# Optimization experiments

Hardware: AMD Instinct MI355X
Metric: run time of the kernel (lower is better)

The kernel has to match this reference:

```python
import jax, jax.numpy as jnp
import numpy as np

NUM_HEADS = 12


def setup_inputs() -> dict:
    key = jax.random.key(0)
    ks = jax.random.split(key, 9)
    R, C, B, E = 128, 256, 1, 768
    s = 1.0 / np.sqrt(E)
    return {
        "x": jax.random.normal(ks[0], (R, C, B, E), jnp.float32),
        "wq": jax.random.normal(ks[1], (E, E), jnp.float32) * s,
        "bq": jax.random.normal(ks[2], (E,), jnp.float32) * 0.02,
        "wk": jax.random.normal(ks[3], (E, E), jnp.float32) * s,
        "bk": jax.random.normal(ks[4], (E,), jnp.float32) * 0.02,
        "wv": jax.random.normal(ks[5], (E, E), jnp.float32) * s,
        "bv": jax.random.normal(ks[6], (E,), jnp.float32) * 0.02,
        "wo": jax.random.normal(ks[7], (E, E), jnp.float32) * s,
        "bo": jax.random.normal(ks[8], (E,), jnp.float32) * 0.02,
    }


def reference(x, wq, bq, wk, bk, wv, bv, wo, bo):
    R, C, B, E = x.shape
    H = NUM_HEADS
    D = E // H
    # scaling = head_dim^-0.5 / sqrt(num_rows)  (tied row attention)
    scaling = (D ** -0.5) / jnp.sqrt(jnp.asarray(R, x.dtype))
    q = (x @ wq + bq).reshape(R, C, B, H, D) * scaling
    k = (x @ wk + bk).reshape(R, C, B, H, D)
    v = (x @ wv + bv).reshape(R, C, B, H, D)
    # tied attention: contract QK^T over rows as well as head_dim
    attn_weights = jnp.einsum('ribhd,rjbhd->hbij', q, k)
    attn_probs = jax.nn.softmax(attn_weights, axis=-1)
    # same probs reused for every row
    context = jnp.einsum('hbij,rjbhd->ribhd', attn_probs, v)
    context = context.reshape(R, C, B, E)
    output = context @ wo + bo
    return (output, attn_probs)
```

## Files before the change

### kernel.cpp

```cpp
#include <hip/hip_runtime.h>
#include <hip/hip_bf16.h>
#include <stdint.h>

typedef __attribute__((ext_vector_type(4))) float f32x4;
typedef __attribute__((ext_vector_type(8))) short bf16x8;

__device__ __forceinline__ unsigned short f2bf(float f) {
  union { float f; unsigned u; } v; v.f = f;
  unsigned r = v.u + 0x7fffu + ((v.u >> 16) & 1u);
  return (unsigned short)(r >> 16);
}

#define GLL16(g, l)                                                   \
  __builtin_amdgcn_global_load_lds(                                   \
      (__attribute__((address_space(1))) void*)(g),                   \
      (__attribute__((address_space(3))) void*)(l), 16, 0, 0)

__global__ __launch_bounds__(256) void k_conv_x(const float* __restrict__ x,
                                                unsigned short* __restrict__ xb) {
  int i = blockIdx.x * 256 + threadIdx.x;
  float4 v = ((const float4*)x)[i];
  ushort4 o;
  o.x = f2bf(v.x); o.y = f2bf(v.y); o.z = f2bf(v.z); o.w = f2bf(v.w);
  ((ushort4*)xb)[i] = o;
}

__global__ __launch_bounds__(256) void k_conv_wT(const float* __restrict__ wq,
                                                 const float* __restrict__ wk,
                                                 const float* __restrict__ wv,
                                                 const float* __restrict__ wo,
                                                 unsigned short* __restrict__ WT) {
  __shared__ unsigned short tile[32][33];
  int t = blockIdx.z;
  const float* w = (t == 0) ? wq : (t == 1) ? wk : (t == 2) ? wv : wo;
  int k0 = blockIdx.x * 32, n0 = blockIdx.y * 32;
  int tx = threadIdx.x, ty = threadIdx.y;
#pragma unroll
  for (int s = 0; s < 32; s += 8)
    tile[tx][ty + s] = f2bf(w[(size_t)(k0 + ty + s) * 768 + n0 + tx]);
  __syncthreads();
#pragma unroll
  for (int s = 0; s < 32; s += 8)
    WT[(size_t)t * 589824 + (size_t)(n0 + ty + s) * 768 + k0 + tx] = tile[ty + s][tx];
}

__device__ __forceinline__ void gemm256_core(const char* __restrict__ Ag,
                                             const char* __restrict__ Bg,
                                             char* lds, int tid,
                                             f32x4 (&acc)[8][4]) {
  const int lane = tid & 63, w = tid >> 6;
  const int wm = w >> 2, wn = w & 3;
  const int fr = lane & 15, kb = (lane >> 4) * 16;
  const bool stageB = (w >= 4);
  const char* Sg = stageB ? Bg : Ag;
  const int wrow0 = 64 * (w & 3);
  const int srow = lane >> 2;
  const int slotL = lane & 3;

#pragma unroll
  for (int t = 0; t < 3; ++t) {
    char* dslot = lds + t * 32768 + (stageB ? 16384 : 0);
#pragma unroll
    for (int c = 0; c < 4; ++c) {
      int row = wrow0 + c * 16 + srow;
      int sG = slotL ^ ((row >> 1) & 3);
      GLL16(Sg + (size_t)row * 1536 + t * 64 + sG * 16,
            dslot + (wrow0 + c * 16) * 64);
    }
  }

  for (int t = 0; t < 24; ++t) {
    if (t < 22)       asm volatile("s_waitcnt vmcnt(8)" ::: "memory");
    else if (t == 22) asm volatile("s_waitcnt vmcnt(4)" ::: "memory");
    else              asm volatile("s_waitcnt vmcnt(0)" ::: "memory");
    __builtin_amdgcn_s_barrier();

    const char* slot = lds + (t & 3) * 32768;
    bf16x8 af[8], bfr[4];
#pragma unroll
    for (int fm = 0; fm < 8; ++fm) {
      int row = wm * 128 + fm * 16 + fr;
      af[fm] = *(const bf16x8*)(slot + row * 64 + (kb ^ (((row >> 1) & 3) << 4)));
    }
#pragma unroll
    for (int fn = 0; fn < 4; ++fn) {
      int row = wn * 64 + fn * 16 + fr;
      bfr[fn] = *(const bf16x8*)(slot + 16384 + row * 64 + (kb ^ (((row >> 1) & 3) << 4)));
    }

    if (t + 3 < 24) {
      char* dslot = lds + ((t + 3) & 3) * 32768 + (stageB ? 16384 : 0);
#pragma unroll
      for (int c = 0; c < 4; ++c) {
        int row = wrow0 + c * 16 + srow;
        int sG = slotL ^ ((row >> 1) & 3);
        GLL16(Sg + (size_t)row * 1536 + (t + 3) * 64 + sG * 16,
              dslot + (wrow0 + c * 16) * 64);
      }
    }

    __builtin_amdgcn_s_setprio(1);
#pragma unroll
    for (int fm = 0; fm < 8; ++fm)
#pragma unroll
      for (int fn = 0; fn < 4; ++fn)
        acc[fm][fn] = __builtin_amdgcn_mfma_f32_16x16x32_bf16(af[fm], bfr[fn],
                                                              acc[fm][fn], 0, 0, 0);
    __builtin_amdgcn_s_setprio(0);
  }
}

__global__ __launch_bounds__(512, 1) void k_gemm_qkv(const unsigned short* __restrict__ Xb,
                                                     const unsigned short* __restrict__ WT,
                                                     const float* __restrict__ bq,
                                                     const float* __restrict__ bk_,
                                                     const float* __restrict__ bv,
                                                     unsigned short* __restrict__ Q,
                                                     unsigned short* __restrict__ K,
                                                     unsigned short* __restrict__ V,
                                                     float qscale) {
  __shared__ __align__(16) char lds[131072];
  const int tid = threadIdx.x, lane = tid & 63, w = tid >> 6;
  const int bid = blockIdx.x;
  const int swz = (bid & 7) * 144 + (bid >> 3);
  const int mt = swz / 9, nt = swz % 9;
  const int m0 = mt * 256;
  const int t = nt / 3, n0 = (nt % 3) * 256;

  const unsigned short* Wt = WT + (size_t)t * 589824;
  const float* bias = (t == 0) ? bq : (t == 1) ? bk_ : bv;
  unsigned short* Out = (t == 0) ? Q : (t == 1) ? K : V;
  const float scale = (t == 0) ? qscale : 1.0f;

  f32x4 acc[8][4];
#pragma unroll
  for (int a = 0; a < 8; ++a)
#pragma unroll
    for (int b = 0; b < 4; ++b) acc[a][b] = (f32x4){0.f, 0.f, 0.f, 0.f};

  gemm256_core((const char*)Xb + (size_t)m0 * 1536,
               (const char*)Wt + (size_t)n0 * 1536, lds, tid, acc);

  const int wm = w >> 2, wn = w & 3;
  const int fr = lane & 15, rowb = (lane >> 4) * 4;
#pragma unroll
  for (int fm = 0; fm < 8; ++fm)
#pragma unroll
    for (int fn = 0; fn < 4; ++fn) {
      int col = n0 + wn * 64 + fn * 16 + fr;
      float b = bias[col];
#pragma unroll
      for (int rg = 0; rg < 4; ++rg) {
        int row = m0 + wm * 128 + fm * 16 + rowb + rg;
        Out[(size_t)row * 768 + col] = f2bf((acc[fm][fn][rg] + b) * scale);
      }
    }
}

__global__ __launch_bounds__(512, 1) void k_gemm_out(const unsigned short* __restrict__ Cb,
                                                     const unsigned short* __restrict__ WTo,
                                                     const float* __restrict__ bo,
                                                     float* __restrict__ Outp) {
  __shared__ __align__(16) char lds[131072];
  const int tid = threadIdx.x, lane = tid & 63, w = tid >> 6;
  const int bid = blockIdx.x;
  const int swz = (bid & 7) * 48 + (bid >> 3);
  const int mt = swz / 3, nt = swz % 3;
  const int m0 = mt * 256, n0 = nt * 256;

  f32x4 acc[8][4];
#pragma unroll
  for (int a = 0; a < 8; ++a)
#pragma unroll
    for (int b = 0; b < 4; ++b) acc[a][b] = (f32x4){0.f, 0.f, 0.f, 0.f};

  gemm256_core((const char*)Cb + (size_t)m0 * 1536,
               (const char*)WTo + (size_t)n0 * 1536, lds, tid, acc);

  const int wm = w >> 2, wn = w & 3;
  const int fr = lane & 15, rowb = (lane >> 4) * 4;
#pragma unroll
  for (int fm = 0; fm < 8; ++fm)
#pragma unroll
    for (int fn = 0; fn < 4; ++fn) {
      int col = n0 + wn * 64 + fn * 16 + fr;
      float b = bo[col];
#pragma unroll
      for (int rg = 0; rg < 4; ++rg) {
        int row = m0 + wm * 128 + fm * 16 + rowb + rg;
        Outp[(size_t)row * 768 + col] = acc[fm][fn][rg] + b;
      }
    }
}

__global__ __launch_bounds__(256) void k_attn(const unsigned short* __restrict__ Q,
                                              const unsigned short* __restrict__ Kb,
                                              float* __restrict__ logits) {
  __shared__ __align__(16) unsigned short As[128 * 64];
  __shared__ __align__(16) unsigned short Bs[128 * 64];
  const int tid = threadIdx.x, lane = tid & 63, w = tid >> 6;
  const int bid = blockIdx.x;
  const int tile = bid & 3;
  const int h = (bid >> 2) % 12;
  const int rs = bid / 48;
  const int i0 = (tile >> 1) * 128, j0 = (tile & 1) * 128;
  const int wm = w >> 1, wn = w & 1;
  const int rl8 = lane >> 3, cb8 = (lane & 7) * 16;
  const int fr = lane & 15, kb = (lane >> 4) * 16;

  f32x4 acc[4][4];
#pragma unroll
  for (int a = 0; a < 4; ++a)
#pragma unroll
    for (int b = 0; b < 4; ++b) acc[a][b] = (f32x4){0.f, 0.f, 0.f, 0.f};

  for (int rr = 0; rr < 16; ++rr) {
    int r = rs * 16 + rr;
    __syncthreads();
#pragma unroll
    for (int c = 0; c < 4; ++c) {
      int row = w * 32 + c * 8 + rl8;
      GLL16((const char*)Q + (size_t)(r * 256 + i0 + row) * 1536 + h * 128 + cb8,
            (char*)As + w * 4096 + c * 1024);
      GLL16((const char*)Kb + (size_t)(r * 256 + j0 + row) * 1536 + h * 128 + cb8,
            (char*)Bs + w * 4096 + c * 1024);
    }
    __syncthreads();
#pragma unroll
    for (int kk = 0; kk < 2; ++kk) {
      bf16x8 af[4], bfr[4];
#pragma unroll
      for (int fm = 0; fm < 4; ++fm)
        af[fm] = *(const bf16x8*)((const char*)As + (wm * 64 + fm * 16 + fr) * 128 + kk * 64 + kb);
#pragma unroll
      for (int fn = 0; fn < 4; ++fn)
        bfr[fn] = *(const bf16x8*)((const char*)Bs + (wn * 64 + fn * 16 + fr) * 128 + kk * 64 + kb);
#pragma unroll
      for (int fm = 0; fm < 4; ++fm)
#pragma unroll
        for (int fn = 0; fn < 4; ++fn)
          acc[fm][fn] = __builtin_amdgcn_mfma_f32_16x16x32_bf16(af[fm], bfr[fn],
                                                                acc[fm][fn], 0, 0, 0);
    }
  }

  float* lg = logits + (size_t)h * 65536;
  const int rowb = (lane >> 4) * 4;
#pragma unroll
  for (int fm = 0; fm < 4; ++fm)
#pragma unroll
    for (int fn = 0; fn < 4; ++fn) {
      int jj = j0 + wn * 64 + fn * 16 + fr;
#pragma unroll
      for (int rg = 0; rg < 4; ++rg) {
        int ii = i0 + wm * 64 + fm * 16 + rowb + rg;
        atomicAdd(&lg[ii * 256 + jj], acc[fm][fn][rg]);
      }
    }
}

__global__ __launch_bounds__(256) void k_softmax(const float* __restrict__ lg,
                                                 float* __restrict__ pout,
                                                 unsigned short* __restrict__ pbf) {
  const int row = blockIdx.x;
  const int j = threadIdx.x;
  const int lane = j & 63, wv = j >> 6;
  float v = lg[(size_t)row * 256 + j];
  float m = v;
#pragma unroll
  for (int o = 32; o; o >>= 1) m = fmaxf(m, __shfl_xor(m, o, 64));
  __shared__ float sm[4], ss[4];
  if (lane == 0) sm[wv] = m;
  __syncthreads();
  m = fmaxf(fmaxf(sm[0], sm[1]), fmaxf(sm[2], sm[3]));
  float e = __expf(v - m);
  float s = e;
#pragma unroll
  for (int o = 32; o; o >>= 1) s += __shfl_xor(s, o, 64);
  if (lane == 0) ss[wv] = s;
  __syncthreads();
  s = ss[0] + ss[1] + ss[2] + ss[3];
  float p = e / s;
  pout[(size_t)row * 256 + j] = p;
  pbf[(size_t)row * 256 + j] = f2bf(p);
}

__global__ __launch_bounds__(256) void k_pv(const unsigned short* __restrict__ P,
                                            const unsigned short* __restrict__ V,
                                            unsigned short* __restrict__ Cb) {
  __shared__ __align__(16) unsigned short Ps[256 * 32];
  __shared__ __align__(16) unsigned short Vs[32 * 64];
  const int tid = threadIdx.x, lane = tid & 63, w = tid >> 6;
  const int bid = blockIdx.x;
  const int h = bid % 12, r = bid / 12;
  const int fr = lane & 15, kb = (lane >> 4) * 16;
  const int rl4 = lane >> 2, cb4 = (lane & 3) * 16;
  const int rl8 = lane >> 3, cb8 = (lane & 7) * 16;

  f32x4 acc[4][4];
#pragma unroll
  for (int a = 0; a < 4; ++a)
#pragma unroll
    for (int b = 0; b < 4; ++b) acc[a][b] = (f32x4){0.f, 0.f, 0.f, 0.f};

  const char* Ph = (const char*)P + (size_t)h * 131072;
  for (int j0 = 0; j0 < 256; j0 += 32) {
    __syncthreads();
#pragma unroll
    for (int c = 0; c < 4; ++c) {
      int row = w * 64 + c * 16 + rl4;
      GLL16(Ph + (size_t)row * 512 + j0 * 2 + cb4, (char*)Ps + w * 4096 + c * 1024);
    }
    {
      int row = w * 8 + rl8;
      GLL16((const char*)V + (size_t)(r * 256 + j0 + row) * 1536 + h * 128 + cb8,
            (char*)Vs + w * 1024);
    }
    __syncthreads();
    bf16x8 af[4];
#pragma unroll
    for (int fm = 0; fm < 4; ++fm)
      af[fm] = *(const bf16x8*)((const char*)Ps + (w * 64 + fm * 16 + fr) * 64 + kb);
#pragma unroll
    for (int fn = 0; fn < 4; ++fn) {
      bf16x8 bvv;
#pragma unroll
      for (int e = 0; e < 8; ++e)
        bvv[e] = (short)Vs[(8 * (lane >> 4) + e) * 64 + fn * 16 + fr];
#pragma unroll
      for (int fm = 0; fm < 4; ++fm)
        acc[fm][fn] = __builtin_amdgcn_mfma_f32_16x16x32_bf16(af[fm], bvv,
                                                              acc[fm][fn], 0, 0, 0);
    }
  }

  const int rowb = (lane >> 4) * 4;
#pragma unroll
  for (int fm = 0; fm < 4; ++fm)
#pragma unroll
    for (int fn = 0; fn < 4; ++fn) {
      int col = h * 64 + fn * 16 + fr;
#pragma unroll
      for (int rg = 0; rg < 4; ++rg) {
        int m = r * 256 + w * 64 + fm * 16 + rowb + rg;
        Cb[(size_t)m * 768 + col] = f2bf(acc[fm][fn][rg]);
      }
    }
}

extern "C" void kernel_launch(void* const* d_in, const int* in_sizes, int n_in,
                              void* d_out, int out_size, void* d_ws, size_t ws_size,
                              hipStream_t stream) {
  const float* x  = (const float*)d_in[0];
  const float* wq = (const float*)d_in[1];
  const float* bq = (const float*)d_in[2];
  const float* wk = (const float*)d_in[3];
  const float* bk = (const float*)d_in[4];
  const float* wv = (const float*)d_in[5];
  const float* bv = (const float*)d_in[6];
  const float* wo = (const float*)d_in[7];
  const float* bo = (const float*)d_in[8];
  float* out = (float*)d_out;

  char* wsb = (char*)d_ws;
  unsigned short* Cb = (unsigned short*)(wsb + 0);
  unsigned short* Qb = (unsigned short*)(wsb + 50331648);
  unsigned short* Kb = (unsigned short*)(wsb + 100663296);
  unsigned short* Vb = (unsigned short*)(wsb + 150994944);
  unsigned short* WT = (unsigned short*)(wsb + 201326592);
  float*          Lg = (float*)(wsb + 206045184);
  unsigned short* Pb = (unsigned short*)(wsb + 209190912);

  const float qscale = 0.011048543456039806f;

  k_conv_x<<<24576, 256, 0, stream>>>(x, Cb);
  k_conv_wT<<<dim3(24, 24, 4), dim3(32, 8), 0, stream>>>(wq, wk, wv, wo, WT);
  k_gemm_qkv<<<1152, 512, 0, stream>>>(Cb, WT, bq, bk, bv, Qb, Kb, Vb, qscale);
  hipMemsetAsync(Lg, 0, (size_t)12 * 256 * 256 * 4, stream);
  k_attn<<<384, 256, 0, stream>>>(Qb, Kb, Lg);
  k_softmax<<<3072, 256, 0, stream>>>(Lg, out + 25165824, Pb);
  k_pv<<<1536, 256, 0, stream>>>(Pb, Vb, Cb);
  k_gemm_out<<<384, 512, 0, stream>>>(Cb, WT + (size_t)3 * 589824, bo, out);
}
```

Measured before the change: 286.2 us.

## Restructure GEMM core into 8-phase pipeline with 128-wide K tiles

Replaces the 4-slot, 64-byte-K software pipeline in the shared 256x256 GEMM core with a double-buffered scheme using 128-byte (64-element) K tiles. Each K tile is split into four phases that interleave LDS fragment reads, staggered global-to-LDS staging of the next A and B tiles, and MFMA bursts, separated by barriers. A uses a permuted row mapping and both operands use a new XOR swizzle. The aim is to halve the number of K iterations and overlap memory traffic with compute more finely, at the cost of more barriers per tile and more register pressure from holding B fragments.

New measurement: 292.9 us. 1.02x slower.

```diff
diff --git a/kernel.cpp b/kernel.cpp
--- a/kernel.cpp
+++ b/kernel.cpp
@@ -44,69 +44,103 @@
     WT[(size_t)t * 589824 + (size_t)(n0 + ty + s) * 768 + k0 + tx] = tile[ty + s][tx];
 }
 
-__device__ __forceinline__ void gemm256_core(const char* __restrict__ Ag,
-                                             const char* __restrict__ Bg,
-                                             char* lds, int tid,
-                                             f32x4 (&acc)[8][4]) {
+__device__ __forceinline__ void gemm256_8p(const char* __restrict__ Ag,
+                                           const char* __restrict__ Bg,
+                                           char* lds, int tid,
+                                           f32x4 (&acc)[8][4]) {
   const int lane = tid & 63, w = tid >> 6;
   const int wm = w >> 2, wn = w & 3;
-  const int fr = lane & 15, kb = (lane >> 4) * 16;
-  const bool stageB = (w >= 4);
-  const char* Sg = stageB ? Bg : Ag;
-  const int wrow0 = 64 * (w & 3);
-  const int srow = lane >> 2;
-  const int slotL = lane & 3;
-
-#pragma unroll
-  for (int t = 0; t < 3; ++t) {
-    char* dslot = lds + t * 32768 + (stageB ? 16384 : 0);
-#pragma unroll
-    for (int c = 0; c < 4; ++c) {
-      int row = wrow0 + c * 16 + srow;
-      int sG = slotL ^ ((row >> 1) & 3);
-      GLL16(Sg + (size_t)row * 1536 + t * 64 + sG * 16,
-            dslot + (wrow0 + c * 16) * 64);
-    }
+  const int fr = lane & 15;
+  const int l3 = lane >> 3;
+  const int chunk = (lane & 7) ^ l3;
+  const int rslot = lane >> 4;
+  const int sw = lane & 7;
+
+  auto stageA = [&](char* Abuf, int half, int kt) {
+#pragma unroll
+    for (int l = 0; l < 2; ++l) {
+      int rbase = half * 128 + l * 64 + w * 8;
+      int rho = rbase + l3;
+      int gr = ((rho >> 6) & 1) * 128 + ((rho >> 7) * 4 + ((rho >> 4) & 3)) * 16
+               + (rho & 15);
+      GLL16(Ag + (size_t)gr * 1536 + kt * 128 + chunk * 16, Abuf + rbase * 128);
+    }
+  };
+  auto stageB = [&](char* Bbuf, int half, int kt) {
+#pragma unroll
+    for (int l = 0; l < 2; ++l) {
+      int rbase = half * 128 + l * 64 + w * 8;
+      int rho = rbase + l3;
+      GLL16(Bg + (size_t)rho * 1536 + kt * 128 + chunk * 16, Bbuf + rbase * 128);
+    }
+  };
+  auto rdA = [&](const char* Abuf, int fm, int kk) -> bf16x8 {
+    int rho = (fm >= 4 ? 128 : 0) + wm * 64 + (fm & 3) * 16 + fr;
+    int slot = (kk * 4 + rslot) ^ sw;
+    return *(const bf16x8*)(Abuf + rho * 128 + slot * 16);
+  };
+  auto rdB = [&](const char* Bbuf, int fn, int kk) -> bf16x8 {
+    int rho = wn * 64 + fn * 16 + fr;
+    int slot = (kk * 4 + rslot) ^ sw;
+    return *(const bf16x8*)(Bbuf + rho * 128 + slot * 16);
+  };
+
+  {
+    char* A0b = lds;          char* B0b = lds + 32768;
+    char* A1b = lds + 65536;  char* B1b = lds + 98304;
+    stageA(A0b, 0, 0); stageA(A0b, 1, 0);
+    stageB(B0b, 0, 0); stageB(B0b, 1, 0);
+    stageB(B1b, 0, 1); stageB(B1b, 1, 1);
+    asm volatile("s_waitcnt vmcnt(4)" ::: "memory");
+    __builtin_amdgcn_s_barrier();
   }
 
-  for (int t = 0; t < 24; ++t) {
-    if (t < 22)       asm volatile("s_waitcnt vmcnt(8)" ::: "memory");
-    else if (t == 22) asm volatile("s_waitcnt vmcnt(4)" ::: "memory");
-    else              asm volatile("s_waitcnt vmcnt(0)" ::: "memory");
-    __builtin_amdgcn_s_barrier();
-
-    const char* slot = lds + (t & 3) * 32768;
-    bf16x8 af[8], bfr[4];
-#pragma unroll
-    for (int fm = 0; fm < 8; ++fm) {
-      int row = wm * 128 + fm * 16 + fr;
-      af[fm] = *(const bf16x8*)(slot + row * 64 + (kb ^ (((row >> 1) & 3) << 4)));
-    }
-#pragma unroll
-    for (int fn = 0; fn < 4; ++fn) {
-      int row = wn * 64 + fn * 16 + fr;
-      bfr[fn] = *(const bf16x8*)(slot + 16384 + row * 64 + (kb ^ (((row >> 1) & 3) << 4)));
-    }
-
-    if (t + 3 < 24) {
-      char* dslot = lds + ((t + 3) & 3) * 32768 + (stageB ? 16384 : 0);
-#pragma unroll
-      for (int c = 0; c < 4; ++c) {
-        int row = wrow0 + c * 16 + srow;
-        int sG = slotL ^ ((row >> 1) & 3);
-        GLL16(Sg + (size_t)row * 1536 + (t + 3) * 64 + sG * 16,
-              dslot + (wrow0 + c * 16) * 64);
-      }
-    }
-
-    __builtin_amdgcn_s_setprio(1);
-#pragma unroll
-    for (int fm = 0; fm < 8; ++fm)
-#pragma unroll
-      for (int fn = 0; fn < 4; ++fn)
-        acc[fm][fn] = __builtin_amdgcn_mfma_f32_16x16x32_bf16(af[fm], bfr[fn],
-                                                              acc[fm][fn], 0, 0, 0);
-    __builtin_amdgcn_s_setprio(0);
+  bf16x8 bfr[4][2];
+#pragma unroll 2
+  for (int kt = 0; kt < 12; ++kt) {
+    const int b = kt & 1;
+    char* Ab = lds + b * 65536;
+    char* Bb = Ab + 32768;
+    char* Ao = lds + (b ^ 1) * 65536;
+
+#pragma unroll
+    for (int q = 0; q < 4; ++q) {
+      bf16x8 af[2][2];
+#pragma unroll
+      for (int fl = 0; fl < 2; ++fl)
+#pragma unroll
+        for (int kk = 0; kk < 2; ++kk) af[fl][kk] = rdA(Ab, 2 * q + fl, kk);
+      if (q == 0) {
+#pragma unroll
+        for (int fn = 0; fn < 4; ++fn)
+#pragma unroll
+          for (int kk = 0; kk < 2; ++kk) bfr[fn][kk] = rdB(Bb, fn, kk);
+      }
+      if (q == 0 && kt + 1 < 12) { stageA(Ao, 0, kt + 1); stageA(Ao, 1, kt + 1); }
+      if (q == 1 && kt + 2 < 12) stageB(Bb, 0, kt + 2);
+      if (q == 2 && kt + 2 < 12) stageB(Bb, 1, kt + 2);
+
+      __builtin_amdgcn_s_barrier();
+      asm volatile("s_waitcnt lgkmcnt(0)" ::: "memory");
+      __builtin_amdgcn_sched_barrier(0);
+
+      __builtin_amdgcn_s_setprio(1);
+#pragma unroll
+      for (int fl = 0; fl < 2; ++fl)
+#pragma unroll
+        for (int fn = 0; fn < 4; ++fn)
+#pragma unroll
+          for (int kk = 0; kk < 2; ++kk)
+            acc[2 * q + fl][fn] = __builtin_amdgcn_mfma_f32_16x16x32_bf16(
+                af[fl][kk], bfr[fn][kk], acc[2 * q + fl][fn], 0, 0, 0);
+      __builtin_amdgcn_s_setprio(0);
+
+      if (q == 3) {
+        if (kt < 10)       asm volatile("s_waitcnt vmcnt(4)" ::: "memory");
+        else if (kt == 10) asm volatile("s_waitcnt vmcnt(0)" ::: "memory");
+      }
+      __builtin_amdgcn_s_barrier();
+    }
   }
 }
 
@@ -138,8 +172,8 @@
 #pragma unroll
     for (int b = 0; b < 4; ++b) acc[a][b] = (f32x4){0.f, 0.f, 0.f, 0.f};
 
-  gemm256_core((const char*)Xb + (size_t)m0 * 1536,
-               (const char*)Wt + (size_t)n0 * 1536, lds, tid, acc);
+  gemm256_8p((const char*)Xb + (size_t)m0 * 1536,
+             (const char*)Wt + (size_t)n0 * 1536, lds, tid, acc);
 
   const int wm = w >> 2, wn = w & 3;
   const int fr = lane & 15, rowb = (lane >> 4) * 4;
@@ -174,8 +208,8 @@
 #pragma unroll
     for (int b = 0; b < 4; ++b) acc[a][b] = (f32x4){0.f, 0.f, 0.f, 0.f};
 
-  gemm256_core((const char*)Cb + (size_t)m0 * 1536,
-               (const char*)WTo + (size_t)n0 * 1536, lds, tid, acc);
+  gemm256_8p((const char*)Cb + (size_t)m0 * 1536,
+             (const char*)WTo + (size_t)n0 * 1536, lds, tid, acc);
 
   const int wm = w >> 2, wn = w & 3;
   const int fr = lane & 15, rowb = (lane >> 4) * 4;
```

## Fuse fp32-to-bf16 conversion of x into the QKV GEMM loader

Applied to the files above, without the earlier changes.

Removes the separate x conversion kernel and has the QKV GEMM stream fp32 x tiles straight into LDS, converting them to bf16 in registers with packed convert instructions before the MFMAs. A new core with a 3-slot pipeline and a swizzled fp32 A layout replaces the bf16 loader for this GEMM. This avoids a full read-write pass over the 100MB activation and its bf16 copy. In exchange, A-tile traffic per GEMM doubles, since each x tile is reread in fp32 by the nine N-tiles, LDS use grows to 144KB, and conversion ALU work is added to the inner loop.

Result: slower. 345.8 us (+20.8%).

```diff
diff --git a/kernel.cpp b/kernel.cpp
--- a/kernel.cpp
+++ b/kernel.cpp
@@ -11,19 +11,19 @@
   return (unsigned short)(r >> 16);
 }
 
+__device__ __forceinline__ bf16x8 cvt8(f32x4 lo, f32x4 hi) {
+  union { bf16x8 v; unsigned u[4]; } r;
+  asm("v_cvt_pk_bf16_f32 %0, %1, %2" : "=v"(r.u[0]) : "v"(lo[0]), "v"(lo[1]));
+  asm("v_cvt_pk_bf16_f32 %0, %1, %2" : "=v"(r.u[1]) : "v"(lo[2]), "v"(lo[3]));
+  asm("v_cvt_pk_bf16_f32 %0, %1, %2" : "=v"(r.u[2]) : "v"(hi[0]), "v"(hi[1]));
+  asm("v_cvt_pk_bf16_f32 %0, %1, %2" : "=v"(r.u[3]) : "v"(hi[2]), "v"(hi[3]));
+  return r.v;
+}
+
 #define GLL16(g, l)                                                   \
   __builtin_amdgcn_global_load_lds(                                   \
       (__attribute__((address_space(1))) void*)(g),                   \
       (__attribute__((address_space(3))) void*)(l), 16, 0, 0)
-
-__global__ __launch_bounds__(256) void k_conv_x(const float* __restrict__ x,
-                                                unsigned short* __restrict__ xb) {
-  int i = blockIdx.x * 256 + threadIdx.x;
-  float4 v = ((const float4*)x)[i];
-  ushort4 o;
-  o.x = f2bf(v.x); o.y = f2bf(v.y); o.z = f2bf(v.z); o.w = f2bf(v.w);
-  ((ushort4*)xb)[i] = o;
-}
 
 __global__ __launch_bounds__(256) void k_conv_wT(const float* __restrict__ wq,
                                                  const float* __restrict__ wk,
@@ -42,6 +42,81 @@
 #pragma unroll
   for (int s = 0; s < 32; s += 8)
     WT[(size_t)t * 589824 + (size_t)(n0 + ty + s) * 768 + k0 + tx] = tile[ty + s][tx];
+}
+
+__device__ __forceinline__ void gemm256f_core(const char* __restrict__ Ag,
+                                              const char* __restrict__ Bg,
+                                              char* lds, int tid,
+                                              f32x4 (&acc)[8][4]) {
+  const int lane = tid & 63, w = tid >> 6;
+  const int wm = w >> 2, wn = w & 3;
+  const int fr = lane & 15, kb = (lane >> 4) * 16;
+  const int c0 = (lane >> 4) * 2;
+  const bool isB = (w >= 4);
+  const int wrow0 = 64 * (w & 3);
+  const int al8 = lane >> 3, ac = (lane & 7) ^ al8;
+  const int srow = lane >> 2, slotL = lane & 3;
+
+  auto stage = [&](int t) {
+    char* base = lds + (t % 3) * 49152;
+    if (!isB) {
+      const char* src = Ag + (size_t)t * 128;
+#pragma unroll
+      for (int c = 0; c < 8; ++c) {
+        int rb = wrow0 + c * 8;
+        GLL16(src + (size_t)(rb + al8) * 3072 + ac * 16, base + rb * 128);
+      }
+    } else {
+      const char* src = Bg + (size_t)t * 64;
+      char* dst = base + 32768;
+#pragma unroll
+      for (int c = 0; c < 4; ++c) {
+        int row = wrow0 + c * 16 + srow;
+        int sG = slotL ^ ((row >> 1) & 3);
+        GLL16(src + (size_t)row * 1536 + sG * 16, dst + (wrow0 + c * 16) * 64);
+      }
+    }
+  };
+
+  stage(0); stage(1);
+
+  for (int t = 0; t < 24; ++t) {
+    if (t < 23) {
+      if (!isB) asm volatile("s_waitcnt vmcnt(8)" ::: "memory");
+      else      asm volatile("s_waitcnt vmcnt(4)" ::: "memory");
+    } else {
+      asm volatile("s_waitcnt vmcnt(0)" ::: "memory");
+    }
+    __builtin_amdgcn_s_barrier();
+
+    const char* base = lds + (t % 3) * 49152;
+    const char* slotB = base + 32768;
+    bf16x8 af[8], bfr[4];
+#pragma unroll
+    for (int fm = 0; fm < 8; ++fm) {
+      int rho = wm * 128 + fm * 16 + fr;
+      int s = rho & 7;
+      f32x4 lo = *(const f32x4*)(base + rho * 128 + ((c0 ^ s) * 16));
+      f32x4 hi = *(const f32x4*)(base + rho * 128 + (((c0 + 1) ^ s) * 16));
+      af[fm] = cvt8(lo, hi);
+    }
+#pragma unroll
+    for (int fn = 0; fn < 4; ++fn) {
+      int row = wn * 64 + fn * 16 + fr;
+      bfr[fn] = *(const bf16x8*)(slotB + row * 64 + (kb ^ (((row >> 1) & 3) << 4)));
+    }
+
+    if (t + 2 < 24) stage(t + 2);
+
+    __builtin_amdgcn_s_setprio(1);
+#pragma unroll
+    for (int fm = 0; fm < 8; ++fm)
+#pragma unroll
+      for (int fn = 0; fn < 4; ++fn)
+        acc[fm][fn] = __builtin_amdgcn_mfma_f32_16x16x32_bf16(af[fm], bfr[fn],
+                                                              acc[fm][fn], 0, 0, 0);
+    __builtin_amdgcn_s_setprio(0);
+  }
 }
 
 __device__ __forceinline__ void gemm256_core(const char* __restrict__ Ag,
@@ -110,7 +185,7 @@
   }
 }
 
-__global__ __launch_bounds__(512, 1) void k_gemm_qkv(const unsigned short* __restrict__ Xb,
+__global__ __launch_bounds__(512, 1) void k_gemm_qkv(const float* __restrict__ X,
                                                      const unsigned short* __restrict__ WT,
                                                      const float* __restrict__ bq,
                                                      const float* __restrict__ bk_,
@@ -119,7 +194,7 @@
                                                      unsigned short* __restrict__ K,
                                                      unsigned short* __restrict__ V,
                                                      float qscale) {
-  __shared__ __align__(16) char lds[131072];
+  __shared__ __align__(16) char lds[147456];
   const int tid = threadIdx.x, lane = tid & 63, w = tid >> 6;
   const int bid = blockIdx.x;
   const int swz = (bid & 7) * 144 + (bid >> 3);
@@ -138,8 +213,8 @@
 #pragma unroll
     for (int b = 0; b < 4; ++b) acc[a][b] = (f32x4){0.f, 0.f, 0.f, 0.f};
 
-  gemm256_core((const char*)Xb + (size_t)m0 * 1536,
-               (const char*)Wt + (size_t)n0 * 1536, lds, tid, acc);
+  gemm256f_core((const char*)X + (size_t)m0 * 3072,
+                (const char*)Wt + (size_t)n0 * 1536, lds, tid, acc);
 
   const int wm = w >> 2, wn = w & 3;
   const int fr = lane & 15, rowb = (lane >> 4) * 4;
@@ -373,9 +448,8 @@
 
   const float qscale = 0.011048543456039806f;
 
-  k_conv_x<<<24576, 256, 0, stream>>>(x, Cb);
   k_conv_wT<<<dim3(24, 24, 4), dim3(32, 8), 0, stream>>>(wq, wk, wv, wo, WT);
-  k_gemm_qkv<<<1152, 512, 0, stream>>>(Cb, WT, bq, bk, bv, Qb, Kb, Vb, qscale);
+  k_gemm_qkv<<<1152, 512, 0, stream>>>(x, WT, bq, bk, bv, Qb, Kb, Vb, qscale);
   hipMemsetAsync(Lg, 0, (size_t)12 * 256 * 256 * 4, stream);
   k_attn<<<384, 256, 0, stream>>>(Qb, Kb, Lg);
   k_softmax<<<3072, 256, 0, stream>>>(Lg, out + 25165824, Pb);
```
